# Performance work log

Measured on AMD Instinct MI355X. Metric: run time of the kernel, lower is better.

The kernel has to match this reference:

```python
import jax, jax.numpy as jnp
import numpy as np

B, S, E, H = 2, 2048, 1024, 16
DH = E // H  # 64


def setup_inputs() -> dict:
    key = jax.random.key(0)
    ks = jax.random.split(key, 13)
    s = 1.0 / np.sqrt(E)
    inp = {
        'query': jax.random.normal(ks[0], (B, S, E), jnp.float32),
        'key':   jax.random.normal(ks[1], (B, S, E), jnp.float32),
        'value': jax.random.normal(ks[2], (B, S, E), jnp.float32),
        # nn.Linear weights stored [out, in]
        'Wq': jax.random.uniform(ks[3], (E, E), jnp.float32, -s, s),
        'bq': jax.random.uniform(ks[4], (E,), jnp.float32, -s, s),
        'Wk': jax.random.uniform(ks[5], (E, E), jnp.float32, -s, s),
        'bk': jax.random.uniform(ks[6], (E,), jnp.float32, -s, s),
        'Wv': jax.random.uniform(ks[7], (E, E), jnp.float32, -s, s),
        'bv': jax.random.uniform(ks[8], (E,), jnp.float32, -s, s),
        # 1x1 Conv2d over head channels: weight [H, H] (squeezed from [H,H,1,1]), bias [H]
        'Wc': jax.random.uniform(ks[9], (H, H), jnp.float32, -1.0 / np.sqrt(H), 1.0 / np.sqrt(H)),
        'bc': jax.random.uniform(ks[10], (H,), jnp.float32, -1.0 / np.sqrt(H), 1.0 / np.sqrt(H)),
        'Wo': jax.random.uniform(ks[11], (E, E), jnp.float32, -s, s),
        'bo': jax.random.uniform(ks[12], (E,), jnp.float32, -s, s),
    }
    return inp


def reference(query, key, value, Wq, bq, Wk, bk, Wv, bv, Wc, bc, Wo, bo):
    b, s = query.shape[0], query.shape[1]
    # projections -> (B, H, S, Dh)
    def split_heads(x):
        return x.reshape(b, s, H, DH).transpose(0, 2, 1, 3)
    Q = split_heads(query @ Wq.T + bq)
    K = split_heads(key @ Wk.T + bk)
    V = split_heads(value @ Wv.T + bv)
    # raw scores (B, H, S, S)
    scores = jnp.einsum('bhqd,bhkd->bhqk', Q, K) / np.sqrt(DH).astype(np.float32)
    # 1x1 conv mixes logits across heads: channel-wise matmul + bias
    noise = jnp.einsum('gh,bhqk->bgqk', Wc, scores) + bc[None, :, None, None]
    scores = scores + noise
    weights = jax.nn.softmax(scores, axis=-1)
    out = jnp.einsum('bhqk,bhkd->bhqd', weights, V)  # (B, H, S, Dh)
    out = out.transpose(0, 2, 1, 3).reshape(b, s, E)
    return out @ Wo.T + bo
```

## Files before the change

kernel.cpp:

```cpp
#include <hip/hip_runtime.h>


typedef __attribute__((ext_vector_type(8))) short bf16x8_t;
typedef __attribute__((ext_vector_type(4))) float f32x4_t;

__device__ inline unsigned short f2bf(float f) {
  unsigned u = __builtin_bit_cast(unsigned, f);
  u += 0x7fffu + ((u >> 16) & 1u);
  return (unsigned short)(u >> 16);
}

struct ConvArgs {
  const float* src[7];
  unsigned short* dst[7];
  int n[7];
};

__global__ __launch_bounds__(256) void convert_f32_bf16(ConvArgs a) {
  const int which = blockIdx.y;
  const int i = (blockIdx.x * 256 + threadIdx.x) * 8;
  if (i >= a.n[which]) return;
  const float* s = a.src[which] + i;
  f32x4_t x0 = *(const f32x4_t*)(s);
  f32x4_t x1 = *(const f32x4_t*)(s + 4);
  bf16x8_t o;
#pragma unroll
  for (int j = 0; j < 4; j++) o[j] = (short)f2bf(x0[j]);
#pragma unroll
  for (int j = 0; j < 4; j++) o[4 + j] = (short)f2bf(x1[j]);
  *(bf16x8_t*)(a.dst[which] + i) = o;
}

__global__ __launch_bounds__(256) void gemm_bt(
    const unsigned short* __restrict__ A, const unsigned short* __restrict__ Bt,
    const float* __restrict__ bias, void* __restrict__ C,
    int M, int N, int K, int c_is_f32)
{
  __shared__ unsigned short As[128 * 32];
  __shared__ unsigned short Bs[128 * 32];
  const int t = threadIdx.x;
  const int l = t & 63;
  const int w = t >> 6;
  const int quad = l >> 4, n16 = l & 15;
  const int wm = (w & 1) * 64, wn = (w >> 1) * 64;
  const long m0 = (long)blockIdx.x * 128, n0 = (long)blockIdx.y * 128;

  f32x4_t acc[4][4] = {};

  const unsigned short* gA = A + (m0 + (t >> 2)) * (long)K + (t & 3) * 8;
  const unsigned short* gB = Bt + (n0 + (t >> 2)) * (long)K + (t & 3) * 8;
  const long rowskip = 64l * K;

  for (int kt = 0; kt < K; kt += 32) {
    bf16x8_t ra0 = *(const bf16x8_t*)(gA + kt);
    bf16x8_t ra1 = *(const bf16x8_t*)(gA + kt + rowskip);
    bf16x8_t rb0 = *(const bf16x8_t*)(gB + kt);
    bf16x8_t rb1 = *(const bf16x8_t*)(gB + kt + rowskip);
    __syncthreads();
    *(bf16x8_t*)&As[t * 8] = ra0;
    *(bf16x8_t*)&As[2048 + t * 8] = ra1;
    *(bf16x8_t*)&Bs[t * 8] = rb0;
    *(bf16x8_t*)&Bs[2048 + t * 8] = rb1;
    __syncthreads();
    bf16x8_t af[4], bfr[4];
#pragma unroll
    for (int i = 0; i < 4; i++) {
      af[i]  = *(const bf16x8_t*)&As[(wm + i * 16 + n16) * 32 + quad * 8];
      bfr[i] = *(const bf16x8_t*)&Bs[(wn + i * 16 + n16) * 32 + quad * 8];
    }
#pragma unroll
    for (int mi = 0; mi < 4; mi++)
#pragma unroll
      for (int ni = 0; ni < 4; ni++)
        acc[mi][ni] = __builtin_amdgcn_mfma_f32_16x16x32_bf16(af[mi], bfr[ni], acc[mi][ni], 0, 0, 0);
  }

#pragma unroll
  for (int ni = 0; ni < 4; ni++) {
    const long n = n0 + wn + ni * 16 + n16;
    const float bv = bias[n];
#pragma unroll
    for (int mi = 0; mi < 4; mi++) {
#pragma unroll
      for (int r = 0; r < 4; r++) {
        const long m = m0 + wm + mi * 16 + quad * 4 + r;
        const float v = acc[mi][ni][r] + bv;
        if (c_is_f32) ((float*)C)[m * N + n] = v;
        else ((unsigned short*)C)[m * N + n] = f2bf(v);
      }
    }
  }
}

__global__ __launch_bounds__(256) void transpose_v(
    const unsigned short* __restrict__ V, unsigned short* __restrict__ VT)
{
  __shared__ unsigned short tile[64][72];
  const int t = threadIdx.x;
  const int s0 = blockIdx.x * 64, h = blockIdx.y, b = blockIdx.z;
#pragma unroll
  for (int r = 0; r < 2; r++) {
    const int elem = r * 2048 + t * 8;
    const int s = elem >> 6, d = elem & 63;
    *(bf16x8_t*)&tile[s][d] =
        *(const bf16x8_t*)&V[(size_t)(b * 2048 + s0 + s) * 1024 + h * 64 + d];
  }
  __syncthreads();
#pragma unroll
  for (int r = 0; r < 2; r++) {
    const int elem = r * 2048 + t * 8;
    const int d = elem >> 6, sl = elem & 63;
    bf16x8_t o;
#pragma unroll
    for (int j = 0; j < 8; j++) o[j] = (short)tile[sl + j][d];
    *(bf16x8_t*)&VT[((size_t)(b * 16 + h) * 64 + d) * 2048 + s0 + sl] = o;
  }
}

__global__ __launch_bounds__(1024) void attention_fused(
    const unsigned short* __restrict__ Qb, const unsigned short* __restrict__ Kb,
    const unsigned short* __restrict__ VT, const float* __restrict__ Wc,
    unsigned short* __restrict__ Obuf)
{
  __shared__ unsigned short sraw[512 * 40];
  __shared__ float sprime[16 * 580];
  __shared__ unsigned short pbuf[16][16 * 40];
  __shared__ unsigned short mmat[16 * 32];

  const int t = threadIdx.x;
  const int g = t >> 6, l = t & 63;
  const int quad = l >> 4, n16 = l & 15;
  const int qb = blockIdx.x, b = blockIdx.y;
  const int q0 = qb * 16;

  for (int i = t; i < 512 * 40; i += 1024) sraw[i] = 0;
  if (t < 256) {
    const int gg = t >> 4, hh = t & 15;
    const float v = (((gg == hh) ? 1.0f : 0.0f) + Wc[gg * 16 + hh]) * 0.125f;
    mmat[gg * 32 + hh] = f2bf(v);
  } else if (t < 512) {
    const int t2 = t - 256;
    mmat[(t2 >> 4) * 32 + 16 + (t2 & 15)] = 0;
  }
  __syncthreads();

  const bf16x8_t mfrag = *(const bf16x8_t*)&mmat[n16 * 32 + quad * 8];
  bf16x8_t qf[2];
#pragma unroll
  for (int dr = 0; dr < 2; dr++)
    qf[dr] = *(const bf16x8_t*)&Qb[(size_t)(b * 2048 + q0 + n16) * 1024 + g * 64 + dr * 32 + quad * 8];

  f32x4_t o[4] = {};
  float m_run = -1e30f, l_run = 0.0f;
  const int qrow = l >> 2, kpos = (l & 3) * 8;

  for (int kt = 0; kt < 2048; kt += 32) {
    bf16x8_t kf[2][2], vf[4];
#pragma unroll
    for (int kc = 0; kc < 2; kc++)
#pragma unroll
      for (int dr = 0; dr < 2; dr++)
        kf[kc][dr] = *(const bf16x8_t*)&Kb[(size_t)(b * 2048 + kt + kc * 16 + n16) * 1024
                                           + g * 64 + dr * 32 + quad * 8];
#pragma unroll
    for (int dc = 0; dc < 4; dc++)
      vf[dc] = *(const bf16x8_t*)&VT[((size_t)(b * 16 + g) * 64 + dc * 16 + n16) * 2048
                                      + kt + quad * 8];

    f32x4_t sfrag[2] = {};
#pragma unroll
    for (int kc = 0; kc < 2; kc++)
#pragma unroll
      for (int dr = 0; dr < 2; dr++)
        sfrag[kc] = __builtin_amdgcn_mfma_f32_16x16x32_bf16(qf[dr], kf[kc][dr], sfrag[kc], 0, 0, 0);

#pragma unroll
    for (int kc = 0; kc < 2; kc++)
#pragma unroll
      for (int r = 0; r < 4; r++) {
        const int col = (quad * 4 + r) * 32 + kc * 16 + n16;
        sraw[col * 40 + g] = f2bf(sfrag[kc][r]);
      }
    __syncthreads();

    f32x4_t mixd[2];
#pragma unroll
    for (int c2 = 0; c2 < 2; c2++) {
      const int c = g * 2 + c2;
      const bf16x8_t bb = *(const bf16x8_t*)&sraw[(c * 16 + n16) * 40 + quad * 8];
      f32x4_t z = {};
      mixd[c2] = __builtin_amdgcn_mfma_f32_16x16x32_bf16(mfrag, bb, z, 0, 0, 0);
    }
#pragma unroll
    for (int c2 = 0; c2 < 2; c2++) {
      const int c = g * 2 + c2;
      const int qq = c >> 1;
      const int kk = (c & 1) * 16 + n16;
#pragma unroll
      for (int r = 0; r < 4; r++)
        sprime[(quad * 4 + r) * 580 + qq * 36 + kk] = mixd[c2][r];
    }
    __syncthreads();

    const float* rowp = &sprime[g * 580 + qrow * 36 + kpos];
    const f32x4_t x0 = *(const f32x4_t*)rowp;
    const f32x4_t x1 = *(const f32x4_t*)(rowp + 4);
    float mloc = fmaxf(fmaxf(fmaxf(x0[0], x0[1]), fmaxf(x0[2], x0[3])),
                       fmaxf(fmaxf(x1[0], x1[1]), fmaxf(x1[2], x1[3])));
    mloc = fmaxf(mloc, __shfl_xor(mloc, 1));
    mloc = fmaxf(mloc, __shfl_xor(mloc, 2));
    const float mnew = fmaxf(m_run, mloc);
    const float alpha = __expf(m_run - mnew);
    float sum = 0.0f;
    bf16x8_t pv8;
#pragma unroll
    for (int j = 0; j < 4; j++) {
      const float e = __expf(x0[j] - mnew);
      sum += e; pv8[j] = (short)f2bf(e);
    }
#pragma unroll
    for (int j = 0; j < 4; j++) {
      const float e = __expf(x1[j] - mnew);
      sum += e; pv8[4 + j] = (short)f2bf(e);
    }
    sum += __shfl_xor(sum, 1);
    sum += __shfl_xor(sum, 2);
    l_run = l_run * alpha + sum;
    m_run = mnew;
    *(bf16x8_t*)&pbuf[g][qrow * 40 + kpos] = pv8;

#pragma unroll
    for (int r = 0; r < 4; r++) {
      const float ar = __shfl(alpha, (quad * 4 + r) * 4);
#pragma unroll
      for (int dc = 0; dc < 4; dc++) o[dc][r] *= ar;
    }

    const bf16x8_t pf = *(const bf16x8_t*)&pbuf[g][n16 * 40 + quad * 8];
#pragma unroll
    for (int dc = 0; dc < 4; dc++)
      o[dc] = __builtin_amdgcn_mfma_f32_16x16x32_bf16(pf, vf[dc], o[dc], 0, 0, 0);
  }

  float linv[4];
#pragma unroll
  for (int r = 0; r < 4; r++)
    linv[r] = 1.0f / __shfl(l_run, (quad * 4 + r) * 4);
#pragma unroll
  for (int dc = 0; dc < 4; dc++)
#pragma unroll
    for (int r = 0; r < 4; r++) {
      const float v = o[dc][r] * linv[r];
      Obuf[(size_t)(b * 2048 + q0 + quad * 4 + r) * 1024 + g * 64 + dc * 16 + n16] = f2bf(v);
    }
}

extern "C" void kernel_launch(void* const* d_in, const int* in_sizes, int n_in,
                              void* d_out, int out_size, void* d_ws, size_t ws_size,
                              hipStream_t stream) {
  const float* query = (const float*)d_in[0];
  const float* key   = (const float*)d_in[1];
  const float* value = (const float*)d_in[2];
  const float* Wq = (const float*)d_in[3];
  const float* bq = (const float*)d_in[4];
  const float* Wk = (const float*)d_in[5];
  const float* bk = (const float*)d_in[6];
  const float* Wv = (const float*)d_in[7];
  const float* bv = (const float*)d_in[8];
  const float* Wc = (const float*)d_in[9];
  const float* Wo = (const float*)d_in[11];
  const float* bo = (const float*)d_in[12];

  char* ws = (char*)d_ws;
  const size_t MB = 1024 * 1024;
  unsigned short* q_bf  = (unsigned short*)(ws);
  unsigned short* k_bf  = (unsigned short*)(ws + 8 * MB);
  unsigned short* v_bf  = (unsigned short*)(ws + 16 * MB);
  unsigned short* wq_bf = (unsigned short*)(ws + 24 * MB);
  unsigned short* wk_bf = (unsigned short*)(ws + 26 * MB);
  unsigned short* wv_bf = (unsigned short*)(ws + 28 * MB);
  unsigned short* wo_bf = (unsigned short*)(ws + 30 * MB);
  unsigned short* Qb    = (unsigned short*)(ws + 32 * MB);
  unsigned short* Kb    = (unsigned short*)(ws + 40 * MB);
  unsigned short* Vb    = (unsigned short*)(ws + 48 * MB);
  unsigned short* VT   = k_bf;
  unsigned short* Obuf = q_bf;

  ConvArgs ca;
  ca.src[0] = query; ca.dst[0] = q_bf;  ca.n[0] = 2 * 2048 * 1024;
  ca.src[1] = key;   ca.dst[1] = k_bf;  ca.n[1] = 2 * 2048 * 1024;
  ca.src[2] = value; ca.dst[2] = v_bf;  ca.n[2] = 2 * 2048 * 1024;
  ca.src[3] = Wq;    ca.dst[3] = wq_bf; ca.n[3] = 1024 * 1024;
  ca.src[4] = Wk;    ca.dst[4] = wk_bf; ca.n[4] = 1024 * 1024;
  ca.src[5] = Wv;    ca.dst[5] = wv_bf; ca.n[5] = 1024 * 1024;
  ca.src[6] = Wo;    ca.dst[6] = wo_bf; ca.n[6] = 1024 * 1024;
  convert_f32_bf16<<<dim3(2048, 7), 256, 0, stream>>>(ca);

  gemm_bt<<<dim3(32, 8), 256, 0, stream>>>(q_bf, wq_bf, bq, Qb, 4096, 1024, 1024, 0);
  gemm_bt<<<dim3(32, 8), 256, 0, stream>>>(k_bf, wk_bf, bk, Kb, 4096, 1024, 1024, 0);
  gemm_bt<<<dim3(32, 8), 256, 0, stream>>>(v_bf, wv_bf, bv, Vb, 4096, 1024, 1024, 0);

  transpose_v<<<dim3(32, 16, 2), 256, 0, stream>>>(Vb, VT);

  attention_fused<<<dim3(128, 2), 1024, 0, stream>>>(Qb, Kb, VT, Wc, Obuf);

  gemm_bt<<<dim3(32, 8), 256, 0, stream>>>(Obuf, wo_bf, bo, d_out, 4096, 1024, 1024, 1);
}
```

Measured before the change: 493.3 us.

## Restructure fused attention loop: prefetch K, softmax in mixing layout, XCD-aware mapping

The head-mixing MFMA output is now consumed directly in registers for the online softmax, which removes the fp32 sprime round-trip through LDS and one barrier per iteration. The QK stage for the next tile is software-pipelined with a prefetch of K, and the sraw layout uses a swizzled slot instead of zero padding. Blocks are remapped to a 1D grid so that each XCD handles one batch and a contiguous range of query blocks, aiming for better L2 reuse of K and V. In exchange, register pressure rises and per-row max and sum state now goes through LDS buffers.

```diff
diff --git a/kernel.cpp b/kernel.cpp
--- a/kernel.cpp
+++ b/kernel.cpp
@@ -2,6 +2,7 @@
 
 
 typedef __attribute__((ext_vector_type(8))) short bf16x8_t;
+typedef __attribute__((ext_vector_type(4))) short bf16x4_t;
 typedef __attribute__((ext_vector_type(4))) float f32x4_t;
 
 __device__ inline unsigned short f2bf(float f) {
@@ -122,130 +123,166 @@
     const unsigned short* __restrict__ VT, const float* __restrict__ Wc,
     unsigned short* __restrict__ Obuf)
 {
-  __shared__ unsigned short sraw[512 * 40];
-  __shared__ float sprime[16 * 580];
-  __shared__ unsigned short pbuf[16][16 * 40];
-  __shared__ unsigned short mmat[16 * 32];
+  __shared__ unsigned short sraw[512 * 36];
+  __shared__ unsigned short pbuf2[16 * 580];
+  __shared__ float alphabuf[256];
+  __shared__ float lbuf[256];
+  __shared__ unsigned short mmat[256];
 
   const int t = threadIdx.x;
   const int g = t >> 6, l = t & 63;
   const int quad = l >> 4, n16 = l & 15;
-  const int qb = blockIdx.x, b = blockIdx.y;
+
+  const int id = blockIdx.x;
+  const int xcd = id & 7;
+  const int b = xcd >> 2;
+  const int qb = (xcd & 3) * 32 + (id >> 3);
   const int q0 = qb * 16;
 
-  for (int i = t; i < 512 * 40; i += 1024) sraw[i] = 0;
   if (t < 256) {
-    const int gg = t >> 4, hh = t & 15;
-    const float v = (((gg == hh) ? 1.0f : 0.0f) + Wc[gg * 16 + hh]) * 0.125f;
-    mmat[gg * 32 + hh] = f2bf(v);
-  } else if (t < 512) {
-    const int t2 = t - 256;
-    mmat[(t2 >> 4) * 32 + 16 + (t2 & 15)] = 0;
+    const float v = ((((t >> 4) == (t & 15)) ? 1.0f : 0.0f) + Wc[t]) * 0.125f;
+    mmat[t] = f2bf(v);
   }
   __syncthreads();
 
-  const bf16x8_t mfrag = *(const bf16x8_t*)&mmat[n16 * 32 + quad * 8];
+  bf16x8_t mfrag;
+  if (quad < 2) mfrag = *(const bf16x8_t*)&mmat[n16 * 16 + quad * 8];
+  else { bf16x8_t z = {0, 0, 0, 0, 0, 0, 0, 0}; mfrag = z; }
+  const int c7 = g >> 2;
+
   bf16x8_t qf[2];
 #pragma unroll
   for (int dr = 0; dr < 2; dr++)
     qf[dr] = *(const bf16x8_t*)&Qb[(size_t)(b * 2048 + q0 + n16) * 1024 + g * 64 + dr * 32 + quad * 8];
 
+  const int slot = g ^ (quad << 3);
+  const unsigned short* kptr = Kb + (size_t)(b * 2048 + n16) * 1024 + g * 64 + quad * 8;
+  const unsigned short* vptr = VT + ((size_t)(b * 16 + g) * 64 + n16) * 2048 + quad * 8;
+
+  bf16x8_t kf[2][2], vf[4];
+  auto load_kf = [&](int kt) {
+#pragma unroll
+    for (int kc = 0; kc < 2; kc++)
+#pragma unroll
+      for (int dr = 0; dr < 2; dr++)
+        kf[kc][dr] = *(const bf16x8_t*)(kptr + (size_t)(kt + kc * 16) * 1024 + dr * 32);
+  };
+  auto load_vf = [&](int kt) {
+#pragma unroll
+    for (int dc = 0; dc < 4; dc++)
+      vf[dc] = *(const bf16x8_t*)(vptr + (size_t)dc * 16 * 2048 + kt);
+  };
+  auto qk_stage = [&]() {
+    f32x4_t sf[2] = {};
+#pragma unroll
+    for (int kc = 0; kc < 2; kc++)
+#pragma unroll
+      for (int dr = 0; dr < 2; dr++)
+        sf[kc] = __builtin_amdgcn_mfma_f32_16x16x32_bf16(qf[dr], kf[kc][dr], sf[kc], 0, 0, 0);
+#pragma unroll
+    for (int kc = 0; kc < 2; kc++)
+#pragma unroll
+      for (int r = 0; r < 4; r++)
+        sraw[((quad * 4 + r) * 32 + kc * 16 + n16) * 36 + slot] = f2bf(sf[kc][r]);
+  };
+
+  load_kf(0);
+  qk_stage();
+  __syncthreads();
+
   f32x4_t o[4] = {};
-  float m_run = -1e30f, l_run = 0.0f;
-  const int qrow = l >> 2, kpos = (l & 3) * 8;
-
-  for (int kt = 0; kt < 2048; kt += 32) {
-    bf16x8_t kf[2][2], vf[4];
-#pragma unroll
-    for (int kc = 0; kc < 2; kc++)
-#pragma unroll
-      for (int dr = 0; dr < 2; dr++)
-        kf[kc][dr] = *(const bf16x8_t*)&Kb[(size_t)(b * 2048 + kt + kc * 16 + n16) * 1024
-                                           + g * 64 + dr * 32 + quad * 8];
-#pragma unroll
-    for (int dc = 0; dc < 4; dc++)
-      vf[dc] = *(const bf16x8_t*)&VT[((size_t)(b * 16 + g) * 64 + dc * 16 + n16) * 2048
-                                      + kt + quad * 8];
-
-    f32x4_t sfrag[2] = {};
-#pragma unroll
-    for (int kc = 0; kc < 2; kc++)
-#pragma unroll
-      for (int dr = 0; dr < 2; dr++)
-        sfrag[kc] = __builtin_amdgcn_mfma_f32_16x16x32_bf16(qf[dr], kf[kc][dr], sfrag[kc], 0, 0, 0);
-
-#pragma unroll
-    for (int kc = 0; kc < 2; kc++)
-#pragma unroll
-      for (int r = 0; r < 4; r++) {
-        const int col = (quad * 4 + r) * 32 + kc * 16 + n16;
-        sraw[col * 40 + g] = f2bf(sfrag[kc][r]);
-      }
-    __syncthreads();
+  float m_run[4], l_run[4];
+#pragma unroll
+  for (int r = 0; r < 4; r++) { m_run[r] = -1e30f; l_run[r] = 0.0f; }
+
+  for (int it = 0; it < 64; ++it) {
+    const int kt = it * 32;
+    load_vf(kt);
+    if (it < 63) load_kf(kt + 32);
 
     f32x4_t mixd[2];
 #pragma unroll
     for (int c2 = 0; c2 < 2; c2++) {
       const int c = g * 2 + c2;
-      const bf16x8_t bb = *(const bf16x8_t*)&sraw[(c * 16 + n16) * 40 + quad * 8];
+      const unsigned short* sp = &sraw[(c * 16 + n16) * 36 + (((quad & 1) ^ c7) << 3)];
+      bf16x4_t lo = *(const bf16x4_t*)sp;
+      bf16x4_t hi = *(const bf16x4_t*)(sp + 4);
+      bf16x8_t bb = {lo[0], lo[1], lo[2], lo[3], hi[0], hi[1], hi[2], hi[3]};
       f32x4_t z = {};
       mixd[c2] = __builtin_amdgcn_mfma_f32_16x16x32_bf16(mfrag, bb, z, 0, 0, 0);
     }
-#pragma unroll
-    for (int c2 = 0; c2 < 2; c2++) {
-      const int c = g * 2 + c2;
-      const int qq = c >> 1;
-      const int kk = (c & 1) * 16 + n16;
-#pragma unroll
-      for (int r = 0; r < 4; r++)
-        sprime[(quad * 4 + r) * 580 + qq * 36 + kk] = mixd[c2][r];
+
+    float p0[4], p1[4], al[4];
+#pragma unroll
+    for (int r = 0; r < 4; r++) {
+      float mx = fmaxf(mixd[0][r], mixd[1][r]);
+      mx = fmaxf(mx, __shfl_xor(mx, 1));
+      mx = fmaxf(mx, __shfl_xor(mx, 2));
+      mx = fmaxf(mx, __shfl_xor(mx, 4));
+      mx = fmaxf(mx, __shfl_xor(mx, 8));
+      const float mnew = fmaxf(m_run[r], mx);
+      al[r] = __expf(m_run[r] - mnew);
+      m_run[r] = mnew;
+      p0[r] = __expf(mixd[0][r] - mnew);
+      p1[r] = __expf(mixd[1][r] - mnew);
+      l_run[r] = l_run[r] * al[r] + (p0[r] + p1[r]);
+    }
+
+    const bool evn = (n16 & 1) == 0;
+#pragma unroll
+    for (int r = 0; r < 4; r++) {
+      const float p0n = __shfl_xor(p0[r], 1);
+      const float p1n = __shfl_xor(p1[r], 1);
+      const float va = evn ? p0[r] : p1n;
+      const float vb = evn ? p0n : p1[r];
+      unsigned pk;
+      asm volatile("v_cvt_pk_bf16_f32 %0, %1, %2" : "=v"(pk) : "v"(va), "v"(vb));
+      const int keven = evn ? n16 : (15 + n16);
+      *(unsigned*)&pbuf2[(quad * 4 + r) * 580 + g * 36 + keven] = pk;
+    }
+    if (n16 == 0) {
+#pragma unroll
+      for (int r = 0; r < 4; r++) alphabuf[(quad * 4 + r) * 16 + g] = al[r];
     }
     __syncthreads();
 
-    const float* rowp = &sprime[g * 580 + qrow * 36 + kpos];
-    const f32x4_t x0 = *(const f32x4_t*)rowp;
-    const f32x4_t x1 = *(const f32x4_t*)(rowp + 4);
-    float mloc = fmaxf(fmaxf(fmaxf(x0[0], x0[1]), fmaxf(x0[2], x0[3])),
-                       fmaxf(fmaxf(x1[0], x1[1]), fmaxf(x1[2], x1[3])));
-    mloc = fmaxf(mloc, __shfl_xor(mloc, 1));
-    mloc = fmaxf(mloc, __shfl_xor(mloc, 2));
-    const float mnew = fmaxf(m_run, mloc);
-    const float alpha = __expf(m_run - mnew);
-    float sum = 0.0f;
-    bf16x8_t pv8;
-#pragma unroll
-    for (int j = 0; j < 4; j++) {
-      const float e = __expf(x0[j] - mnew);
-      sum += e; pv8[j] = (short)f2bf(e);
-    }
-#pragma unroll
-    for (int j = 0; j < 4; j++) {
-      const float e = __expf(x1[j] - mnew);
-      sum += e; pv8[4 + j] = (short)f2bf(e);
-    }
-    sum += __shfl_xor(sum, 1);
-    sum += __shfl_xor(sum, 2);
-    l_run = l_run * alpha + sum;
-    m_run = mnew;
-    *(bf16x8_t*)&pbuf[g][qrow * 40 + kpos] = pv8;
-
 #pragma unroll
     for (int r = 0; r < 4; r++) {
-      const float ar = __shfl(alpha, (quad * 4 + r) * 4);
+      const float ar = alphabuf[g * 16 + quad * 4 + r];
 #pragma unroll
       for (int dc = 0; dc < 4; dc++) o[dc][r] *= ar;
     }
-
-    const bf16x8_t pf = *(const bf16x8_t*)&pbuf[g][n16 * 40 + quad * 8];
+    const unsigned short* pp = &pbuf2[g * 580 + n16 * 36 + quad * 8];
+    bf16x4_t plo = *(const bf16x4_t*)pp;
+    bf16x4_t phi = *(const bf16x4_t*)(pp + 4);
+    bf16x8_t pf = {plo[0], plo[1], plo[2], plo[3], phi[0], phi[1], phi[2], phi[3]};
 #pragma unroll
     for (int dc = 0; dc < 4; dc++)
       o[dc] = __builtin_amdgcn_mfma_f32_16x16x32_bf16(pf, vf[dc], o[dc], 0, 0, 0);
-  }
-
+
+    if (it < 63) {
+      qk_stage();
+      __syncthreads();
+    }
+  }
+
+#pragma unroll
+  for (int r = 0; r < 4; r++) {
+    float s = l_run[r];
+    s += __shfl_xor(s, 1);
+    s += __shfl_xor(s, 2);
+    s += __shfl_xor(s, 4);
+    s += __shfl_xor(s, 8);
+    l_run[r] = s;
+  }
+  if (n16 == 0) {
+#pragma unroll
+    for (int r = 0; r < 4; r++) lbuf[(quad * 4 + r) * 16 + g] = l_run[r];
+  }
+  __syncthreads();
   float linv[4];
 #pragma unroll
-  for (int r = 0; r < 4; r++)
-    linv[r] = 1.0f / __shfl(l_run, (quad * 4 + r) * 4);
+  for (int r = 0; r < 4; r++) linv[r] = 1.0f / lbuf[g * 16 + quad * 4 + r];
 #pragma unroll
   for (int dc = 0; dc < 4; dc++)
 #pragma unroll
@@ -302,7 +339,7 @@
 
   transpose_v<<<dim3(32, 16, 2), 256, 0, stream>>>(Vb, VT);
 
-  attention_fused<<<dim3(128, 2), 1024, 0, stream>>>(Qb, Kb, VT, Wc, Obuf);
+  attention_fused<<<dim3(256), 1024, 0, stream>>>(Qb, Kb, VT, Wc, Obuf);
 
   gemm_bt<<<dim3(32, 8), 256, 0, stream>>>(Obuf, wo_bf, bo, d_out, 4096, 1024, 1024, 1);
 }
```

New measurement: 479.4 us. 1.03x faster.
